# Performance work log

Hardware: AMD Instinct MI355X
Metric: run time of the kernel (lower is better)

Reference implementation:

```python
import jax, jax.numpy as jnp
import numpy as np

INPUT_SLICE = (1, 1, 2, 4)   # MSB -> LSB bit widths, total 8 bits (two's complement)
WEIGHT_SLICE = (1, 1, 2, 4)
IN_FEATURES = 2048
OUT_FEATURES = 2048
M_TOKENS = 2048


def _slice_quant(x, bits):
    """Quantize x to INT-(sum(bits)) two's complement and split into bit-plane slices.

    Returns (planes [n_slices, *x.shape], shift_weights [n_slices], scale scalar).
    Reconstruction: sum_i shift_weights[i] * planes[i] == round(x/scale), MSB plane
    carries the sign (two's-complement weighting).
    """
    bits = np.asarray(bits)
    total = int(bits.sum())
    qmax = float(2 ** (total - 1) - 1)
    scale = jnp.max(jnp.abs(x)) / qmax
    q = jnp.clip(jnp.round(x / scale), -qmax, qmax)
    u = jnp.where(q < 0.0, q + 2.0 ** total, q)  # unsigned two's-complement repr
    # bit offset of each slice, MSB slice first: e.g. (1,1,2,4) -> shifts (7,6,4,0)
    shifts = np.concatenate([np.cumsum(bits[::-1])[::-1][1:], [0]])
    planes, weights = [], []
    for i, (w, sh) in enumerate(zip(bits, shifts)):
        p = jnp.floor(u / 2.0 ** sh) % 2.0 ** w
        if i == 0:  # MSB slice: its top bit is the sign bit
            p = p - (p >= 2.0 ** (w - 1)) * 2.0 ** w
        planes.append(p)
        weights.append(2.0 ** sh)
    return jnp.stack(planes), jnp.asarray(weights, x.dtype), scale


def setup_inputs() -> dict:
    key = jax.random.key(0)
    kx, kw, kb = jax.random.split(key, 3)
    x = jax.random.normal(kx, (M_TOKENS, IN_FEATURES), dtype=jnp.float32)
    # kaiming-uniform-ish init for weight [out, in], uniform bias bound 1/sqrt(fan_in)
    bound_w = float(np.sqrt(6.0 / ((1 + 5.0) * IN_FEATURES)))
    weight = jax.random.uniform(kw, (OUT_FEATURES, IN_FEATURES), jnp.float32, -bound_w, bound_w)
    bound_b = 1.0 / float(np.sqrt(IN_FEATURES))
    bias = jax.random.uniform(kb, (OUT_FEATURES,), jnp.float32, -bound_b, bound_b)
    return {"x": x, "weight": weight, "bias": bias}


def reference(x, weight, bias):
    # slice input [Si, M, K] and transposed weight [Sw, K, N] into bit planes
    xs, wx, sx = _slice_quant(x, INPUT_SLICE)
    ws, ww, sw = _slice_quant(weight.T, WEIGHT_SLICE)
    # per-slice-pair matmuls recombined with shift weights 2^shift_i * 2^shift_j
    out_q = jnp.einsum("imk,jkn,i,j->mn", xs, ws, wx, ww)
    return out_q * (sx * sw) + bias  # dequantize and add bias
```

## Files before the change

### kernel.cpp

```cpp
#include <hip/hip_runtime.h>
#include <hip/hip_bf16.h>
#include <stdint.h>

typedef int v4i __attribute__((ext_vector_type(4)));

#define M_TOK 2048
#define NFEAT 2048
#define KDIM  2048

__global__ __launch_bounds__(256) void k_absmax(const float4* __restrict__ x,
                                                const float4* __restrict__ w,
                                                float* __restrict__ pmax) {
  const int bid = blockIdx.x, tid = threadIdx.x;
  const int which = bid >> 8;
  const int sub = bid & 255;
  const float4* src = which ? w : x;
  const int n4 = (M_TOK * KDIM) / 4;
  float m = 0.0f;
  for (int i = sub * 256 + tid; i < n4; i += 256 * 256) {
    float4 v = src[i];
    m = fmaxf(m, fmaxf(fmaxf(fabsf(v.x), fabsf(v.y)), fmaxf(fabsf(v.z), fabsf(v.w))));
  }
  #pragma unroll
  for (int o = 32; o; o >>= 1) m = fmaxf(m, __shfl_down(m, o, 64));
  __shared__ float sm[4];
  const int wid = tid >> 6, lane = tid & 63;
  if (lane == 0) sm[wid] = m;
  __syncthreads();
  if (tid == 0) pmax[bid] = fmaxf(fmaxf(sm[0], sm[1]), fmaxf(sm[2], sm[3]));
}

__global__ __launch_bounds__(256) void k_quant(const float4* __restrict__ x,
                                               const float4* __restrict__ w,
                                               char4* __restrict__ qx,
                                               char4* __restrict__ qw,
                                               const float* __restrict__ pmax) {
  const int bid = blockIdx.x, tid = threadIdx.x;
  const int which = bid >> 8;
  const int sub = bid & 255;
  const float4* src = which ? w : x;
  char4* dst = which ? qw : qx;
  __shared__ float sm[4];
  {
    const int wid = tid >> 6, lane = tid & 63;
    float m = pmax[which * 256 + tid];
    #pragma unroll
    for (int o = 32; o; o >>= 1) m = fmaxf(m, __shfl_down(m, o, 64));
    if (lane == 0) sm[wid] = m;
  }
  __syncthreads();
  const float gmax = fmaxf(fmaxf(sm[0], sm[1]), fmaxf(sm[2], sm[3]));
  const float s = gmax / 127.0f;
  const int n4 = (M_TOK * KDIM) / 4;
  for (int i = sub * 256 + tid; i < n4; i += 256 * 256) {
    float4 v = src[i];
    char4 q;
    q.x = (signed char)(int)fminf(127.f, fmaxf(-127.f, rintf(v.x / s)));
    q.y = (signed char)(int)fminf(127.f, fmaxf(-127.f, rintf(v.y / s)));
    q.z = (signed char)(int)fminf(127.f, fmaxf(-127.f, rintf(v.z / s)));
    q.w = (signed char)(int)fminf(127.f, fmaxf(-127.f, rintf(v.w / s)));
    dst[i] = q;
  }
}

__device__ __forceinline__ void gload16(const void* g, void* l) {
  __builtin_amdgcn_global_load_lds(
      (const __attribute__((address_space(1))) uint32_t*)(uintptr_t)g,
      (__attribute__((address_space(3))) uint32_t*)(uint32_t)(uintptr_t)l,
      16, 0, 0);
}

__global__ __launch_bounds__(512, 2) void k_gemm(const signed char* __restrict__ qa,
                                                 const signed char* __restrict__ qb,
                                                 const float* __restrict__ bias,
                                                 const float* __restrict__ pmax,
                                                 float* __restrict__ out) {
  __shared__ __align__(16) signed char ldsA[3][128 * 64];
  __shared__ __align__(16) signed char ldsB[3][128 * 64];
  __shared__ float smx[8], smw[8];
  const int tid = threadIdx.x;
  const int lane = tid & 63, wid = tid >> 6;

  const int bid = (blockIdx.x & 7) * 32 + (blockIdx.x >> 3);
  const int tm = (bid >> 4) * 128;
  const int tn = (bid & 15) * 128;

  const int wm = (wid >> 2) * 64;
  const int wn = (wid & 3) * 32;
  const int kg = lane >> 4, lr = lane & 15;
  const int swz = (kg ^ (lr >> 2)) * 16;

  v4i acc[4][2] = {};

  auto stage = [&](int buf, int kt) {
    const int k0 = kt * 64;
    const int c = tid;
    const int row = c >> 2, kc = (c & 3) ^ ((c >> 4) & 3);
    const int ldsoff = (wid * 64) * 16;
    gload16(qa + (size_t)(tm + row) * KDIM + k0 + kc * 16, &ldsA[buf][ldsoff]);
    gload16(qb + (size_t)(tn + row) * KDIM + k0 + kc * 16, &ldsB[buf][ldsoff]);
  };

  stage(0, 0);
  stage(1, 1);

  const int NKT = KDIM / 64;
  for (int kt = 0; kt < NKT; ++kt) {
    if (kt + 1 < NKT) asm volatile("s_waitcnt vmcnt(2)" ::: "memory");
    else              asm volatile("s_waitcnt vmcnt(0)" ::: "memory");
    __builtin_amdgcn_sched_barrier(0);
    __builtin_amdgcn_s_barrier();
    __builtin_amdgcn_sched_barrier(0);
    if (kt + 2 < NKT) stage((kt + 2) % 3, kt + 2);
    const int cur = kt % 3;
    v4i af[4], bf[2];
    #pragma unroll
    for (int mi = 0; mi < 4; ++mi)
      af[mi] = *(const v4i*)&ldsA[cur][(wm + mi * 16 + lr) * 64 + swz];
    #pragma unroll
    for (int ni = 0; ni < 2; ++ni)
      bf[ni] = *(const v4i*)&ldsB[cur][(wn + ni * 16 + lr) * 64 + swz];
    #pragma unroll
    for (int mi = 0; mi < 4; ++mi)
      #pragma unroll
      for (int ni = 0; ni < 2; ++ni)
        acc[mi][ni] = __builtin_amdgcn_mfma_i32_16x16x64_i8(af[mi], bf[ni], acc[mi][ni], 0, 0, 0);
  }

  {
    const float m0 = pmax[tid & 255], m1 = pmax[256 + (tid & 255)];
    float a = m0, b = m1;
    #pragma unroll
    for (int o = 32; o; o >>= 1) {
      a = fmaxf(a, __shfl_down(a, o, 64));
      b = fmaxf(b, __shfl_down(b, o, 64));
    }
    if (lane == 0) { smx[wid] = a; smw[wid] = b; }
  }
  __syncthreads();
  float gx = smx[0], gw = smw[0];
  #pragma unroll
  for (int j = 1; j < 8; ++j) { gx = fmaxf(gx, smx[j]); gw = fmaxf(gw, smw[j]); }
  const float deq = (gx / 127.0f) * (gw / 127.0f);

  #pragma unroll
  for (int ni = 0; ni < 2; ++ni) {
    const int col = tn + wn + ni * 16 + lr;
    const float bv = bias[col];
    #pragma unroll
    for (int mi = 0; mi < 4; ++mi) {
      const int row0 = tm + wm + mi * 16 + kg * 4;
      #pragma unroll
      for (int r = 0; r < 4; ++r)
        out[(size_t)(row0 + r) * NFEAT + col] = (float)acc[mi][ni][r] * deq + bv;
    }
  }
}

extern "C" void kernel_launch(void* const* d_in, const int* in_sizes, int n_in,
                              void* d_out, int out_size, void* d_ws, size_t ws_size,
                              hipStream_t stream) {
  const float* x    = (const float*)d_in[0];
  const float* w    = (const float*)d_in[1];
  const float* bias = (const float*)d_in[2];
  float* out = (float*)d_out;

  float* pmax = (float*)d_ws;
  signed char* qx = (signed char*)d_ws + 8192;
  signed char* qw = qx + (size_t)M_TOK * KDIM;

  k_absmax<<<dim3(512), 256, 0, stream>>>((const float4*)x, (const float4*)w, pmax);
  k_quant<<<dim3(512), 256, 0, stream>>>(
      (const float4*)x, (const float4*)w, (char4*)qx, (char4*)qw, pmax);
  k_gemm<<<dim3(256), 512, 0, stream>>>(qx, qw, bias, pmax, out);
}
```

Measured before the change: 36.18 us.

## Fuse absmax and quantize kernels with grid-wide spin barrier, keeping inputs in registers

Merges the abs-max reduction and quantization into one kernel. Each block holds its 16 float4 values in registers, publishes its partial max with an atomic store, then spins until every block's partial max is nonzero. This removes the second full read of the fp32 inputs and one kernel launch. In exchange it adds a memset launch and relies on all 512 blocks being co-resident, since otherwise the spin can deadlock. It also assumes every partial max is strictly positive.

```diff
diff --git a/kernel.cpp b/kernel.cpp
--- a/kernel.cpp
+++ b/kernel.cpp
@@ -8,58 +8,65 @@
 #define NFEAT 2048
 #define KDIM  2048
 
-__global__ __launch_bounds__(256) void k_absmax(const float4* __restrict__ x,
-                                                const float4* __restrict__ w,
-                                                float* __restrict__ pmax) {
+__global__ __launch_bounds__(256) void k_maxquant(const float4* __restrict__ x,
+                                                  const float4* __restrict__ w,
+                                                  char4* __restrict__ qx,
+                                                  char4* __restrict__ qw,
+                                                  float* __restrict__ pmax) {
   const int bid = blockIdx.x, tid = threadIdx.x;
-  const int which = bid >> 8;
-  const int sub = bid & 255;
-  const float4* src = which ? w : x;
-  const int n4 = (M_TOK * KDIM) / 4;
+  const int which = bid >> 8, sub = bid & 255;
+  const float4* __restrict__ src = which ? w : x;
+  char4* __restrict__ dst = which ? qw : qx;
+  const int wid = tid >> 6, lane = tid & 63;
+  __shared__ float sm[4];
+
+  float4 v[16];
   float m = 0.0f;
-  for (int i = sub * 256 + tid; i < n4; i += 256 * 256) {
-    float4 v = src[i];
-    m = fmaxf(m, fmaxf(fmaxf(fabsf(v.x), fabsf(v.y)), fmaxf(fabsf(v.z), fabsf(v.w))));
+  #pragma unroll
+  for (int j = 0; j < 16; ++j) {
+    v[j] = src[sub * 256 + tid + j * 65536];
+    m = fmaxf(m, fmaxf(fmaxf(fabsf(v[j].x), fabsf(v[j].y)),
+                       fmaxf(fabsf(v[j].z), fabsf(v[j].w))));
   }
   #pragma unroll
   for (int o = 32; o; o >>= 1) m = fmaxf(m, __shfl_down(m, o, 64));
-  __shared__ float sm[4];
-  const int wid = tid >> 6, lane = tid & 63;
   if (lane == 0) sm[wid] = m;
   __syncthreads();
-  if (tid == 0) pmax[bid] = fmaxf(fmaxf(sm[0], sm[1]), fmaxf(sm[2], sm[3]));
-}
+  if (tid == 0) {
+    const float bm = fmaxf(fmaxf(sm[0], sm[1]), fmaxf(sm[2], sm[3]));
+    __hip_atomic_store(&pmax[bid], bm, __ATOMIC_RELEASE, __HIP_MEMORY_SCOPE_AGENT);
+  }
 
-__global__ __launch_bounds__(256) void k_quant(const float4* __restrict__ x,
-                                               const float4* __restrict__ w,
-                                               char4* __restrict__ qx,
-                                               char4* __restrict__ qw,
-                                               const float* __restrict__ pmax) {
-  const int bid = blockIdx.x, tid = threadIdx.x;
-  const int which = bid >> 8;
-  const int sub = bid & 255;
-  const float4* src = which ? w : x;
-  char4* dst = which ? qw : qx;
-  __shared__ float sm[4];
-  {
-    const int wid = tid >> 6, lane = tid & 63;
-    float m = pmax[which * 256 + tid];
-    #pragma unroll
-    for (int o = 32; o; o >>= 1) m = fmaxf(m, __shfl_down(m, o, 64));
-    if (lane == 0) sm[wid] = m;
+  if (wid == 0) {
+    const int base = which * 256 + lane * 4;
+    for (;;) {
+      float a0 = __hip_atomic_load(&pmax[base + 0], __ATOMIC_RELAXED, __HIP_MEMORY_SCOPE_AGENT);
+      float a1 = __hip_atomic_load(&pmax[base + 1], __ATOMIC_RELAXED, __HIP_MEMORY_SCOPE_AGENT);
+      float a2 = __hip_atomic_load(&pmax[base + 2], __ATOMIC_RELAXED, __HIP_MEMORY_SCOPE_AGENT);
+      float a3 = __hip_atomic_load(&pmax[base + 3], __ATOMIC_RELAXED, __HIP_MEMORY_SCOPE_AGENT);
+      if (__all(fminf(fminf(a0, a1), fminf(a2, a3)) > 0.0f)) break;
+      __builtin_amdgcn_s_sleep(8);
+    }
   }
+  __syncthreads();
+
+  float g = __hip_atomic_load(&pmax[which * 256 + tid], __ATOMIC_RELAXED,
+                              __HIP_MEMORY_SCOPE_AGENT);
+  #pragma unroll
+  for (int o = 32; o; o >>= 1) g = fmaxf(g, __shfl_down(g, o, 64));
+  if (lane == 0) sm[wid] = g;
   __syncthreads();
   const float gmax = fmaxf(fmaxf(sm[0], sm[1]), fmaxf(sm[2], sm[3]));
   const float s = gmax / 127.0f;
-  const int n4 = (M_TOK * KDIM) / 4;
-  for (int i = sub * 256 + tid; i < n4; i += 256 * 256) {
-    float4 v = src[i];
+
+  #pragma unroll
+  for (int j = 0; j < 16; ++j) {
     char4 q;
-    q.x = (signed char)(int)fminf(127.f, fmaxf(-127.f, rintf(v.x / s)));
-    q.y = (signed char)(int)fminf(127.f, fmaxf(-127.f, rintf(v.y / s)));
-    q.z = (signed char)(int)fminf(127.f, fmaxf(-127.f, rintf(v.z / s)));
-    q.w = (signed char)(int)fminf(127.f, fmaxf(-127.f, rintf(v.w / s)));
-    dst[i] = q;
+    q.x = (signed char)(int)fminf(127.f, fmaxf(-127.f, rintf(v[j].x / s)));
+    q.y = (signed char)(int)fminf(127.f, fmaxf(-127.f, rintf(v[j].y / s)));
+    q.z = (signed char)(int)fminf(127.f, fmaxf(-127.f, rintf(v[j].z / s)));
+    q.w = (signed char)(int)fminf(127.f, fmaxf(-127.f, rintf(v[j].w / s)));
+    dst[sub * 256 + tid + j * 65536] = q;
   }
 }
 
@@ -128,8 +135,7 @@
   }
 
   {
-    const float m0 = pmax[tid & 255], m1 = pmax[256 + (tid & 255)];
-    float a = m0, b = m1;
+    float a = pmax[tid & 255], b = pmax[256 + (tid & 255)];
     #pragma unroll
     for (int o = 32; o; o >>= 1) {
       a = fmaxf(a, __shfl_down(a, o, 64));
@@ -169,8 +175,8 @@
   signed char* qx = (signed char*)d_ws + 8192;
   signed char* qw = qx + (size_t)M_TOK * KDIM;
 
-  k_absmax<<<dim3(512), 256, 0, stream>>>((const float4*)x, (const float4*)w, pmax);
-  k_quant<<<dim3(512), 256, 0, stream>>>(
-      (const float4*)x, (const float4*)w, (char4*)qx, (char4*)qw, pmax);
+  hipMemsetAsync(pmax, 0, 512 * sizeof(float), stream);
+  k_maxquant<<<dim3(512), 256, 0, stream>>>((const float4*)x, (const float4*)w,
+                                            (char4*)qx, (char4*)qw, pmax);
   k_gemm<<<dim3(256), 512, 0, stream>>>(qx, qw, bias, pmax, out);
 }
```

After: 53.11 us. 1.47x slower.
